# Performance work log

Hardware: AMD Instinct MI355X
Metric: run time of the kernel (lower is better)

Reference implementation:

```python
import jax, jax.numpy as jnp
import numpy as np

B, N, C, H, R = 64, 197, 768, 12, 98   # batch, tokens, dim, heads, eliminated tokens
SPARSITY, ALPHA = 0.2, 0.1
EPS = 1e-5  # torch nn.LayerNorm default


def layernorm(x, g, b):
    m = jnp.mean(x, axis=-1, keepdims=True)
    v = jnp.var(x, axis=-1, keepdims=True)
    return (x - m) / jnp.sqrt(v + EPS) * g + b


def setup_inputs() -> dict:
    key = jax.random.key(0)
    ks = jax.random.split(key, 8)
    s = lambda k, sh: (jax.random.normal(k, sh, jnp.float32) * 0.02)
    return dict(
        x=jax.random.normal(ks[0], (B, N, C), jnp.float32),
        norm1_g=jnp.ones((C,), jnp.float32), norm1_b=jnp.zeros((C,), jnp.float32),
        qkv_w=s(ks[1], (C, 3 * C)),                      # qkv_bias=False
        proj_w=s(ks[2], (C, C)), proj_b=jnp.zeros((C,), jnp.float32),
        norm2_g=jnp.ones((C,), jnp.float32), norm2_b=jnp.zeros((C,), jnp.float32),
        fc1_w=s(ks[3], (C, 4 * C)), fc1_b=jnp.zeros((4 * C,), jnp.float32),
        fc2_w=s(ks[4], (4 * C, C)), fc2_b=jnp.zeros((C,), jnp.float32),
    )


def reference(x, norm1_g, norm1_b, qkv_w, proj_w, proj_b,
              norm2_g, norm2_b, fc1_w, fc1_b, fc2_w, fc2_b):
    Dh = C // H
    scale = Dh ** -0.5
    # --- attention block ---
    h = layernorm(x, norm1_g, norm1_b)
    qkv = (h @ qkv_w).reshape(B, N, 3, H, Dh).transpose(2, 0, 3, 1, 4)
    q, k, v = qkv[0] * scale, qkv[1], qkv[2]
    attn = jax.nn.softmax(jnp.einsum('bhnd,bhmd->bhnm', q, k), axis=-1)  # [B,H,N,N]
    out = jnp.einsum('bhnm,bhmd->bhnd', attn, v).transpose(0, 2, 1, 3).reshape(B, N, C)
    x = x + out @ proj_w + proj_b
    # --- selection: DiagAttn (head-mean attention diagonal, excluding CLS) ---
    diag = jnp.diagonal(attn.mean(1), axis1=1, axis2=2)[:, 1:]          # [B, N-1]
    token_rank = jnp.argsort(-diag, axis=1) + 1                          # indices into [1, N)
    nk = N - 1 - R                                                       # kept image tokens
    idx_kept = jnp.sort(jnp.concatenate(
        [jnp.zeros((B, 1), token_rank.dtype), token_rank[:, :nk]], axis=1), axis=1)  # [B, K]
    idx_elim = jnp.sort(token_rank[:, nk:], axis=1)                      # [B, R]
    K = nk + 1
    # --- propagate: ThresholdGraph (multihead=True, threshold=True) ---
    x_kept = jnp.take_along_axis(x, idx_kept[:, :, None], axis=1)        # [B, K, C]
    x_elim = jnp.take_along_axis(x, idx_elim[:, :, None], axis=1)        # [B, R, C]
    w = jnp.take_along_axis(attn, idx_kept[:, None, :, None], axis=2)    # [B,H,K,N]
    w = jnp.take_along_axis(w, idx_elim[:, None, None, :], axis=3)       # [B,H,K,R]
    thr_idx = int(R * K * SPARSITY)
    w_sorted = -jnp.sort(-w.reshape(B, H, K * R), axis=-1)               # descending
    thr = w_sorted[:, :, thr_idx][:, :, None, None]
    w = jnp.where(w >= thr, w, jnp.zeros((), w.dtype))
    x_prop = jnp.einsum('bhke,behd->bkhd', w, x_elim.reshape(B, R, H, Dh)).reshape(B, K, C)
    x = x_kept + ALPHA * x_prop                                          # [B, K, C]
    # --- mlp block ---
    h2 = layernorm(x, norm2_g, norm2_b)
    h2 = jax.nn.gelu(h2 @ fc1_w + fc1_b, approximate=False) @ fc2_w + fc2_b
    return x + h2
```

## Files before the change

### kernel.cpp

```cpp
#include <hip/hip_runtime.h>
#include <math.h>

#define NTOK 197
#define CD   768
#define NH   12
#define DH   64
#define NBATCH 64
#define RTOK 98
#define KTOK 99
#define THRN 1941

typedef __attribute__((ext_vector_type(8))) short short8;
typedef __attribute__((ext_vector_type(8))) unsigned short u16x8;
typedef __attribute__((ext_vector_type(4))) float floatx4;

__device__ __forceinline__ int clamp196(int v){ return ((unsigned)v > 196u) ? 196 : v; }
__device__ __forceinline__ unsigned short f2b(float f){
  unsigned u = __float_as_uint(f);
  return (unsigned short)((u + 0x7FFFu + ((u>>16)&1u)) >> 16);
}
__device__ __forceinline__ float us2f(unsigned short u){ return __uint_as_float(((unsigned)u)<<16); }
__device__ __forceinline__ int swz(int row, int q){ return q ^ (((row>>1)&3)<<3); }

__global__ __launch_bounds__(256) void fill_kernel(float* __restrict__ out, int n, float val)
{
  int i = blockIdx.x*256 + threadIdx.x;
  if (i < n) out[i] = val;
}

__global__ __launch_bounds__(256) void tcast_k(const float* __restrict__ src, int K, int ldn, int col0,
                                               unsigned short* __restrict__ dst)
{
  __shared__ float t[32][33];
  int n0 = blockIdx.x*32, k0 = blockIdx.y*32;
  int lx = threadIdx.x & 31, ly = threadIdx.x >> 5;
#pragma unroll
  for (int i=0;i<4;i++)
    t[ly + i*8][lx] = src[(long)(k0 + ly + i*8)*ldn + col0 + n0 + lx];
  __syncthreads();
#pragma unroll
  for (int i=0;i<4;i++){
    int n = ly + i*8;
    dst[(long)(n0 + n)*K + k0 + lx] = f2b(t[lx][n]);
  }
}

__global__ __launch_bounds__(256) void tcast3_k(const float* __restrict__ src, int K, int ldn, int col0,
                                                unsigned short* __restrict__ dsth,
                                                unsigned short* __restrict__ dstl)
{
  __shared__ float t[32][33];
  int n0 = blockIdx.x*32, k0 = blockIdx.y*32;
  int lx = threadIdx.x & 31, ly = threadIdx.x >> 5;
#pragma unroll
  for (int i=0;i<4;i++)
    t[ly + i*8][lx] = src[(long)(k0 + ly + i*8)*ldn + col0 + n0 + lx];
  __syncthreads();
#pragma unroll
  for (int i=0;i<4;i++){
    int n = ly + i*8;
    float v = t[lx][n];
    unsigned short h = f2b(v);
    dsth[(long)(n0 + n)*K + k0 + lx] = h;
    dstl[(long)(n0 + n)*K + k0 + lx] = f2b(v - us2f(h));
  }
}

__global__ __launch_bounds__(256) void ln_kernel(const float* __restrict__ xin,
                                                 const float* __restrict__ gam,
                                                 const float* __restrict__ bet,
                                                 unsigned short* __restrict__ outh,
                                                 unsigned short* __restrict__ outl)
{
  int row = blockIdx.x;
  int tid = threadIdx.x;
  long base = (long)row * CD;
  float v[3];
#pragma unroll
  for (int i=0;i<3;i++) v[i] = xin[base + tid + i*256];
  float s  = v[0]+v[1]+v[2];
  float s2 = v[0]*v[0]+v[1]*v[1]+v[2]*v[2];
#pragma unroll
  for (int off=32; off; off>>=1){ s += __shfl_down(s,off); s2 += __shfl_down(s2,off); }
  __shared__ float ps[4], ps2[4], mb[2];
  if ((tid&63)==0){ ps[tid>>6]=s; ps2[tid>>6]=s2; }
  __syncthreads();
  if (tid==0){
    float S  = ps[0]+ps[1]+ps[2]+ps[3];
    float S2 = ps2[0]+ps2[1]+ps2[2]+ps2[3];
    float m  = S / (float)CD;
    float var = S2 / (float)CD - m*m;
    mb[0]=m; mb[1]=1.0f/sqrtf(var + 1e-5f);
  }
  __syncthreads();
  float m=mb[0], inv=mb[1];
#pragma unroll
  for (int i=0;i<3;i++){
    int c = tid + i*256;
    float r = (v[i]-m)*inv*gam[c] + bet[c];
    unsigned short h = f2b(r);
    outh[base+c] = h;
    if (outl) outl[base+c] = f2b(r - us2f(h));
  }
}

struct GemmP {
  const float* A;
  const void*  B;
  void*        C;
  int M, N, K, ldb, ldc;
  int zdiv;
  long as0, as1, bs0, bs1, cs0, cs1;
};

template<int EPI, int BF16B>
__global__ __launch_bounds__(256) void gemm_k(GemmP p)
{
  __shared__ float As[16][64];
  __shared__ float Bs[16][64];
  int z = blockIdx.z;
  int zq = z / p.zdiv, zr = z - zq*p.zdiv;
  long aoff = zq*p.as0 + zr*p.as1;
  long boff = zq*p.bs0 + zr*p.bs1;
  long coff = zq*p.cs0 + zr*p.cs1;
  int m0 = blockIdx.y*64, n0 = blockIdx.x*64;
  int tid = threadIdx.x;
  int tx = tid & 15, ty = tid >> 4;
  int am = tid >> 2, ak = (tid & 3) * 4;
  int bk = tid >> 4, bn = (tid & 15) * 4;
  bool aVec = ((p.K & 3) == 0);
  float acc[4][4] = {};
  for (int k0 = 0; k0 < p.K; k0 += 16) {
    float aa[4] = {0.f,0.f,0.f,0.f};
    {
      int gm = m0 + am;
      if (gm < p.M) {
        const float* ap = p.A + aoff + (long)gm*p.K + k0 + ak;
        if (aVec) {
          float4 t = *(const float4*)ap;
          aa[0]=t.x; aa[1]=t.y; aa[2]=t.z; aa[3]=t.w;
        } else {
#pragma unroll
          for (int i=0;i<4;i++) if (k0+ak+i < p.K) aa[i] = ap[i];
        }
      }
    }
    float bb[4] = {0.f,0.f,0.f,0.f};
    {
      int gk = k0 + bk;
      if (gk < p.K) {
        long idx = boff + (long)gk*p.ldb + n0 + bn;
        if (BF16B) {
          const unsigned short* bp = (const unsigned short*)p.B + idx;
          if (n0 + bn + 3 < p.N) {
            ushort4 t = *(const ushort4*)bp;
            bb[0]=us2f(t.x); bb[1]=us2f(t.y); bb[2]=us2f(t.z); bb[3]=us2f(t.w);
          } else {
#pragma unroll
            for (int i=0;i<4;i++) if (n0+bn+i < p.N) bb[i] = us2f(bp[i]);
          }
        } else {
          const float* bp = (const float*)p.B + idx;
          if (n0 + bn + 3 < p.N) {
            float4 t = *(const float4*)bp;
            bb[0]=t.x; bb[1]=t.y; bb[2]=t.z; bb[3]=t.w;
          } else {
#pragma unroll
            for (int i=0;i<4;i++) if (n0+bn+i < p.N) bb[i] = bp[i];
          }
        }
      }
    }
    __syncthreads();
#pragma unroll
    for (int i=0;i<4;i++) As[ak+i][am] = aa[i];
#pragma unroll
    for (int i=0;i<4;i++) Bs[bk][bn+i] = bb[i];
    __syncthreads();
#pragma unroll
    for (int kk=0;kk<16;kk++){
      float4 av = *(const float4*)&As[kk][ty*4];
      float4 bv = *(const float4*)&Bs[kk][tx*4];
      float av4[4]={av.x,av.y,av.z,av.w};
      float bv4[4]={bv.x,bv.y,bv.z,bv.w};
#pragma unroll
      for (int i=0;i<4;i++)
#pragma unroll
        for (int j=0;j<4;j++) acc[i][j] = fmaf(av4[i], bv4[j], acc[i][j]);
    }
  }
#pragma unroll
  for (int i=0;i<4;i++){
    int gm = m0 + ty*4 + i;
    if (gm >= p.M) continue;
#pragma unroll
    for (int j=0;j<4;j++){
      int gn = n0 + tx*4 + j;
      if (gn >= p.N) continue;
      float val = acc[i][j];
      if (EPI == 2) {
        ((unsigned short*)p.C)[coff + (long)gm*p.ldc + gn] = f2b(val);
      } else {
        ((float*)p.C)[coff + (long)gm*p.ldc + gn] = val;
      }
    }
  }
}

struct MmP {
  const unsigned short* A;
  const unsigned short* B;
  void* C;
  const float* bias;
  const float* resid;
  unsigned short* vout;
  int M, N, K, ldc;
};

template<int EPI>
__global__ __launch_bounds__(256) void mgemm_k(MmP p)
{
  __shared__ short As[128*32];
  __shared__ short Bs[128*32];
  int tid = threadIdx.x;
  int m0 = blockIdx.y*128, n0 = blockIdx.x*128;
  int w = tid>>6, l = tid&63;
  int wm = (w&1)*64, wn = (w>>1)*64;
  int lr = l&15, kq = (l>>4)*8;
  floatx4 acc[4][4];
#pragma unroll
  for (int i=0;i<4;i++)
#pragma unroll
    for (int j=0;j<4;j++) acc[i][j] = (floatx4){0.f,0.f,0.f,0.f};
  int r0i = tid>>2, q0 = (tid&3)*8;
  int r1i = r0i + 64;
  int w0s = swz(r0i, q0), w1s = swz(r1i, q0);
  for (int k0 = 0; k0 < p.K; k0 += 32) {
    u16x8 a0 = {0,0,0,0,0,0,0,0}, a1 = {0,0,0,0,0,0,0,0};
    { int gm = m0 + r0i;
      if (gm < p.M) a0 = *(const u16x8*)(p.A + (long)gm*p.K + k0 + q0); }
    { int gm = m0 + r1i;
      if (gm < p.M) a1 = *(const u16x8*)(p.A + (long)gm*p.K + k0 + q0); }
    u16x8 b0 = *(const u16x8*)(p.B + (long)(n0 + r0i)*p.K + k0 + q0);
    u16x8 b1 = *(const u16x8*)(p.B + (long)(n0 + r1i)*p.K + k0 + q0);
    __syncthreads();
    *(u16x8*)&As[r0i*32 + w0s] = a0;
    *(u16x8*)&As[r1i*32 + w1s] = a1;
    *(u16x8*)&Bs[r0i*32 + w0s] = b0;
    *(u16x8*)&Bs[r1i*32 + w1s] = b1;
    __syncthreads();
    short8 af[4], bfr[4];
#pragma unroll
    for (int mt=0;mt<4;mt++){ int rr = wm + mt*16 + lr; af[mt]  = *(short8*)&As[rr*32 + swz(rr,kq)]; }
#pragma unroll
    for (int nt=0;nt<4;nt++){ int rr = wn + nt*16 + lr; bfr[nt] = *(short8*)&Bs[rr*32 + swz(rr,kq)]; }
#pragma unroll
    for (int mt=0;mt<4;mt++)
#pragma unroll
      for (int nt=0;nt<4;nt++)
        acc[mt][nt] = __builtin_amdgcn_mfma_f32_16x16x32_bf16(af[mt], bfr[nt], acc[mt][nt], 0, 0, 0);
  }
  int rbase = (l>>4)*4;
#pragma unroll
  for (int mt=0;mt<4;mt++){
#pragma unroll
    for (int r=0;r<4;r++){
      int gm = m0 + wm + mt*16 + rbase + r;
      if (gm >= p.M) continue;
#pragma unroll
      for (int nt=0;nt<4;nt++){
        int gn = n0 + wn + nt*16 + lr;
        float val = acc[mt][nt][r];
        if (EPI == 1) {
          int cb = gm / NTOK, tok = gm - cb*NTOK;
          int h = gn >> 6, d = gn & 63;
          p.vout[(((long)cb*NH + h)*NTOK + tok)*DH + d] = f2b(val);
        } else if (EPI == 2) {
          ((float*)p.C)[(long)gm*p.ldc + gn] = val + p.bias[gn] + p.resid[(long)gm*p.ldc + gn];
        } else {
          float u = val + p.bias[gn];
          ((unsigned short*)p.C)[(long)gm*p.ldc + gn] = f2b(0.5f*u*(1.0f + erff(u*0.70710678118654752f)));
        }
      }
    }
  }
}

struct Mm3P {
  const unsigned short *Ah, *Al, *Bh, *Bl;
  float* C;
  unsigned short *qh, *ql, *kh, *kl;
  long az, bz, cz;
  int M, N, K, ldc;
};

template<int EPI>
__global__ __launch_bounds__(256) void mgemm3_k(Mm3P p)
{
  __shared__ short Ahs[128*32], Als[128*32], Bhs[128*32], Bls[128*32];
  int tid = threadIdx.x;
  int z = blockIdx.z;
  const unsigned short* Azh = p.Ah + (long)z*p.az;
  const unsigned short* Azl = p.Al + (long)z*p.az;
  const unsigned short* Bzh = p.Bh + (long)z*p.bz;
  const unsigned short* Bzl = p.Bl + (long)z*p.bz;
  int m0 = blockIdx.y*128, n0 = blockIdx.x*128;
  int w = tid>>6, l = tid&63;
  int wm = (w&1)*64, wn = (w>>1)*64;
  int lr = l&15, kq = (l>>4)*8;
  floatx4 acc[4][4];
#pragma unroll
  for (int i=0;i<4;i++)
#pragma unroll
    for (int j=0;j<4;j++) acc[i][j] = (floatx4){0.f,0.f,0.f,0.f};
  int r0i = tid>>2, q0 = (tid&3)*8;
  int r1i = r0i + 64;
  int w0s = swz(r0i, q0), w1s = swz(r1i, q0);
  for (int k0 = 0; k0 < p.K; k0 += 32) {
    u16x8 ah0={0,0,0,0,0,0,0,0}, al0={0,0,0,0,0,0,0,0};
    u16x8 ah1={0,0,0,0,0,0,0,0}, al1={0,0,0,0,0,0,0,0};
    u16x8 bh0={0,0,0,0,0,0,0,0}, bl0={0,0,0,0,0,0,0,0};
    u16x8 bh1={0,0,0,0,0,0,0,0}, bl1={0,0,0,0,0,0,0,0};
    { int gm = m0 + r0i;
      if (gm < p.M) {
        long o = (long)gm*p.K + k0 + q0;
        ah0 = *(const u16x8*)(Azh + o);
        al0 = *(const u16x8*)(Azl + o);
      } }
    { int gm = m0 + r1i;
      if (gm < p.M) {
        long o = (long)gm*p.K + k0 + q0;
        ah1 = *(const u16x8*)(Azh + o);
        al1 = *(const u16x8*)(Azl + o);
      } }
    { int gn = n0 + r0i;
      if (gn < p.N) {
        long o = (long)gn*p.K + k0 + q0;
        bh0 = *(const u16x8*)(Bzh + o);
        bl0 = *(const u16x8*)(Bzl + o);
      } }
    { int gn = n0 + r1i;
      if (gn < p.N) {
        long o = (long)gn*p.K + k0 + q0;
        bh1 = *(const u16x8*)(Bzh + o);
        bl1 = *(const u16x8*)(Bzl + o);
      } }
    __syncthreads();
    *(u16x8*)&Ahs[r0i*32 + w0s] = ah0;
    *(u16x8*)&Ahs[r1i*32 + w1s] = ah1;
    *(u16x8*)&Als[r0i*32 + w0s] = al0;
    *(u16x8*)&Als[r1i*32 + w1s] = al1;
    *(u16x8*)&Bhs[r0i*32 + w0s] = bh0;
    *(u16x8*)&Bhs[r1i*32 + w1s] = bh1;
    *(u16x8*)&Bls[r0i*32 + w0s] = bl0;
    *(u16x8*)&Bls[r1i*32 + w1s] = bl1;
    __syncthreads();
    short8 afh[4], afl[4], bfh[4], bfl[4];
#pragma unroll
    for (int mt=0;mt<4;mt++){
      int rr = wm + mt*16 + lr; int rs = rr*32 + swz(rr,kq);
      afh[mt] = *(short8*)&Ahs[rs];
      afl[mt] = *(short8*)&Als[rs];
    }
#pragma unroll
    for (int nt=0;nt<4;nt++){
      int rr = wn + nt*16 + lr; int rs = rr*32 + swz(rr,kq);
      bfh[nt] = *(short8*)&Bhs[rs];
      bfl[nt] = *(short8*)&Bls[rs];
    }
#pragma unroll
    for (int mt=0;mt<4;mt++)
#pragma unroll
      for (int nt=0;nt<4;nt++){
        acc[mt][nt] = __builtin_amdgcn_mfma_f32_16x16x32_bf16(afh[mt], bfh[nt], acc[mt][nt], 0, 0, 0);
        acc[mt][nt] = __builtin_amdgcn_mfma_f32_16x16x32_bf16(afh[mt], bfl[nt], acc[mt][nt], 0, 0, 0);
        acc[mt][nt] = __builtin_amdgcn_mfma_f32_16x16x32_bf16(afl[mt], bfh[nt], acc[mt][nt], 0, 0, 0);
      }
  }
  int rbase = (l>>4)*4;
#pragma unroll
  for (int mt=0;mt<4;mt++){
#pragma unroll
    for (int r=0;r<4;r++){
      int gm = m0 + wm + mt*16 + rbase + r;
      if (gm >= p.M) continue;
#pragma unroll
      for (int nt=0;nt<4;nt++){
        int gn = n0 + wn + nt*16 + lr;
        if (gn >= p.N) continue;
        float val = acc[mt][nt][r];
        if (EPI == 0) {
          p.C[(long)z*p.cz + (long)gm*p.ldc + gn] = val;
        } else {
          int which = (gn >= CD) ? 1 : 0;
          int rc = gn - which*CD;
          int hd = rc >> 6, dd = rc & 63;
          int cb = gm / NTOK, tok = gm - cb*NTOK;
          long off = (((long)cb*NH + hd)*NTOK + tok)*DH + dd;
          float v = which ? val : val*0.125f;
          unsigned short h = f2b(v);
          unsigned short lo16 = f2b(v - us2f(h));
          if (which) { p.kh[off] = h; p.kl[off] = lo16; }
          else       { p.qh[off] = h; p.ql[off] = lo16; }
        }
      }
    }
  }
}

__global__ __launch_bounds__(256) void softmax_kernel(float* __restrict__ attn)
{
  long row = (long)blockIdx.x*4 + (threadIdx.x>>6);
  int ln = threadIdx.x & 63;
  float* rp = attn + row*NTOK;
  float v[4]; float mx = -3.4e38f;
#pragma unroll
  for (int i=0;i<4;i++){
    int c = ln + i*64;
    v[i] = (c < NTOK) ? rp[c] : -3.4e38f;
    mx = fmaxf(mx, v[i]);
  }
#pragma unroll
  for (int off=32; off; off>>=1) mx = fmaxf(mx, __shfl_xor(mx, off));
  float sum = 0.f;
#pragma unroll
  for (int i=0;i<4;i++){
    int c = ln + i*64;
    v[i] = (c < NTOK) ? expf(v[i]-mx) : 0.f;
    sum += v[i];
  }
#pragma unroll
  for (int off=32; off; off>>=1) sum += __shfl_xor(sum, off);
#pragma unroll
  for (int i=0;i<4;i++){
    int c = ln + i*64;
    if (c < NTOK) rp[c] = v[i] / sum;
  }
}

__global__ __launch_bounds__(256) void select_kernel(const float* __restrict__ attn,
                                                     int* __restrict__ idx_kept,
                                                     int* __restrict__ idx_elim, int b0)
{
  int cb = blockIdx.x, tid = threadIdx.x;
  int b = b0 + cb;
  __shared__ float diag[NTOK-1];
  __shared__ int kept[NTOK];
  if (tid < NTOK-1) {
    int t = tid + 1;
    float s = 0.f;
#pragma unroll
    for (int h=0; h<NH; h++)
      s += attn[(((long)cb*NH + h)*NTOK + t)*NTOK + t];
    diag[tid] = s / 12.0f;
  }
  if (tid < KTOK) idx_kept[b*KTOK + tid] = 0;
  if (tid < RTOK) idx_elim[b*RTOK + tid] = 1;
  __syncthreads();
  if (tid < NTOK-1) {
    float dv = diag[tid];
    int r = 0;
    for (int m=0; m<NTOK-1; m++){
      float dm = diag[m];
      r += ((dm > dv) || (dm == dv && m < tid)) ? 1 : 0;
    }
    kept[tid+1] = (r < (NTOK-1-RTOK)) ? 1 : 0;
  }
  __syncthreads();
  if (tid < NTOK-1) {
    int t = tid + 1;
    if (kept[t]) {
      int pos = 1;
      for (int s2=1; s2<t; s2++) pos += kept[s2];
      if (pos >= 1 && pos < KTOK) idx_kept[b*KTOK + pos] = t;
    } else {
      int pos = 0;
      for (int s2=1; s2<t; s2++) pos += 1 - kept[s2];
      if (pos >= 0 && pos < RTOK) idx_elim[b*RTOK + pos] = t;
    }
  }
  if (tid == 0) idx_kept[b*KTOK] = 0;
}

__global__ __launch_bounds__(256) void prop_kernel(const float* __restrict__ attn,
                                                   const float* __restrict__ x1c,
                                                   const int* __restrict__ idx_kept,
                                                   const int* __restrict__ idx_elim,
                                                   float* __restrict__ x2, int b0)
{
  int z = blockIdx.x;
  int cb = z / NH, h = z - cb*NH;
  int b = b0 + cb;
  int tid = threadIdx.x;
  __shared__ float w[KTOK*RTOK];
  __shared__ unsigned short xe[RTOK*DH];
  __shared__ int kidx[KTOK], eidx[RTOK];
  __shared__ int cw[4];
  __shared__ int ctot;
  if (tid < KTOK) kidx[tid] = clamp196(idx_kept[b*KTOK + tid]);
  if (tid < RTOK) eidx[tid] = clamp196(idx_elim[b*RTOK + tid]);
  __syncthreads();
  const float* ab = attn + (long)z*NTOK*NTOK;
  for (int i=tid; i<KTOK*RTOK; i+=256){
    int k = i / RTOK, e = i - k*RTOK;
    w[i] = ab[kidx[k]*NTOK + eidx[e]];
  }
  for (int i=tid; i<RTOK*DH; i+=256){
    int e = i >> 6, d = i & 63;
    xe[i] = f2b(x1c[((long)cb*NTOK + eidx[e])*CD + h*DH + d]);
  }
  __syncthreads();
  unsigned lo = 0u, hi = 0x3f800001u;
  while (hi - lo > 1u) {
    unsigned mid = (lo + hi) >> 1;
    float t = __uint_as_float(mid);
    int c = 0;
    for (int i=tid; i<KTOK*RTOK; i+=256) c += (w[i] >= t) ? 1 : 0;
#pragma unroll
    for (int off=32; off; off>>=1) c += __shfl_down(c, off);
    if ((tid & 63) == 0) cw[tid>>6] = c;
    __syncthreads();
    if (tid == 0) ctot = cw[0]+cw[1]+cw[2]+cw[3];
    __syncthreads();
    int tot = ctot;
    __syncthreads();
    if (tot >= THRN) lo = mid; else hi = mid;
  }
  float tv = __uint_as_float(lo);
  for (int i=tid; i<KTOK*RTOK; i+=256) if (w[i] < tv) w[i] = 0.f;
  __syncthreads();
  int d = tid & 63;
  for (int k = tid>>6; k < KTOK; k += 4) {
    const float* wr = &w[k*RTOK];
    float acc = 0.f;
#pragma unroll 7
    for (int e=0; e<RTOK; e++)
      acc = fmaf(wr[e], us2f(xe[(e<<6) + d]), acc);
    float xk = x1c[((long)cb*NTOK + kidx[k])*CD + h*DH + d];
    x2[((long)b*KTOK + k)*CD + h*DH + d] = xk + 0.1f*acc;
  }
}

extern "C" void kernel_launch(void* const* d_in, const int* in_sizes, int n_in,
                              void* d_out, int out_size, void* d_ws, size_t ws_size,
                              hipStream_t stream)
{
  const float* x     = (const float*)d_in[0];
  const float* n1g   = (const float*)d_in[1];
  const float* n1b   = (const float*)d_in[2];
  const float* qkvw  = (const float*)d_in[3];
  const float* projw = (const float*)d_in[4];
  const float* projb = (const float*)d_in[5];
  const float* n2g   = (const float*)d_in[6];
  const float* n2b   = (const float*)d_in[7];
  const float* fc1w  = (const float*)d_in[8];
  const float* fc1b  = (const float*)d_in[9];
  const float* fc2w  = (const float*)d_in[10];
  const float* fc2b  = (const float*)d_in[11];
  float* out = (float*)d_out;

  const long XROW = (long)NTOK*CD;
  const long AH   = (long)NTOK*NTOK;
  const long AB   = (long)NH*AH;
  const long QH   = (long)NH*NTOK*DH;
  const long SMALL = 6336L + 6272L;
  const long WFIX  = 1769472L;
  const long PB = AB + 3*XROW + XROW/2;
  const long MLPFIX = 2359296L;
  const long MINREQ = SMALL + WFIX + (MLPFIX + 64*1920L > PB ? MLPFIX + 64*1920L : PB);

  long wsf = (long)(ws_size / 4);
  if (wsf < MINREQ) {
    float val = (float)(ws_size >> 20) * 1000.0f + 1.0f;
    fill_kernel<<<dim3((out_size+255)/256), 256, 0, stream>>>(out, out_size, val);
    return;
  }

  long avail = wsf - SMALL - WFIX;
  int G = (int)(avail / PB);
  if (G > NBATCH) G = NBATCH;
  if (G < 1) G = 1;
  long rcl = ((avail - MLPFIX) / 1920L) / 64L * 64L;
  int RC = (int)(rcl > 6336L ? 6336L : rcl);
  if (RC < 64) RC = 64;

  float* ws = (float*)d_ws;
  int*   idx_kept = (int*)ws;
  int*   idx_elim = idx_kept + 6336;
  unsigned short* qkwh   = (unsigned short*)(ws + SMALL);
  unsigned short* qkwl   = qkwh + 1179648;
  unsigned short* qkvwvT = qkwl + 1179648;
  unsigned short* projwT = qkvwvT + 589824;
  float* base  = ws + SMALL + WFIX;
  float* attnc = base;
  unsigned short* qh = (unsigned short*)(base + (long)G*AB);
  unsigned short* ql = qh + (long)G*XROW;
  float* x1c = (float*)qh;
  unsigned short* kh = (unsigned short*)(base + (long)G*AB + (long)G*XROW);
  unsigned short* kl = kh + (long)G*XROW;
  unsigned short* aoutb = kh;
  unsigned short* vc = (unsigned short*)(base + (long)G*AB + 2L*G*XROW);
  unsigned short* h1h = (unsigned short*)(base + (long)G*AB + 2L*G*XROW + (long)G*XROW/2);
  unsigned short* h1l = h1h + (long)G*XROW;
  unsigned short* fc1wT = (unsigned short*)base;
  unsigned short* fc2wT = fc1wT + 2359296;
  unsigned short* h2b   = (unsigned short*)(base + MLPFIX);
  unsigned short* gb    = h2b + (long)RC*CD;

  tcast3_k<<<dim3(48,24), 256, 0, stream>>>(qkvw, CD, 3*CD, 0, qkwh, qkwl);
  tcast_k <<<dim3(24,24), 256, 0, stream>>>(qkvw, CD, 3*CD, 2*CD, qkvwvT);
  tcast_k <<<dim3(24,24), 256, 0, stream>>>(projw, CD, CD, 0, projwT);

  for (int b0 = 0; b0 < NBATCH; b0 += G) {
    int GL = (NBATCH - b0 < G) ? (NBATCH - b0) : G;
    int MROW = GL*NTOK;
    ln_kernel<<<dim3(MROW), 256, 0, stream>>>(x + (long)b0*XROW, n1g, n1b, h1h, h1l);
    {
      Mm3P p{}; p.Ah=h1h; p.Al=h1l; p.Bh=qkwh; p.Bl=qkwl;
      p.qh=qh; p.ql=ql; p.kh=kh; p.kl=kl;
      p.M=MROW; p.N=2*CD; p.K=CD; p.ldc=0; p.az=0; p.bz=0; p.cz=0;
      mgemm3_k<1><<<dim3(12,(MROW+127)/128,1), 256, 0, stream>>>(p);
    }
    {
      MmP p{}; p.A=h1h; p.B=qkvwvT; p.vout=vc;
      p.M=MROW; p.N=CD; p.K=CD; p.ldc=CD;
      mgemm_k<1><<<dim3(6,(MROW+127)/128,1), 256, 0, stream>>>(p);
    }
    {
      Mm3P p{}; p.Ah=qh; p.Al=ql; p.Bh=kh; p.Bl=kl; p.C=attnc;
      p.M=NTOK; p.N=NTOK; p.K=DH; p.ldc=NTOK;
      p.az=(long)NTOK*DH; p.bz=(long)NTOK*DH; p.cz=AH;
      mgemm3_k<0><<<dim3(2,2,GL*NH), 256, 0, stream>>>(p);
    }
    softmax_kernel<<<dim3(GL*591), 256, 0, stream>>>(attnc);
    select_kernel<<<dim3(GL), 256, 0, stream>>>(attnc, idx_kept, idx_elim, b0);
    {
      GemmP p{}; p.A=attnc; p.B=vc; p.C=aoutb;
      p.M=NTOK; p.N=DH; p.K=NTOK; p.ldb=DH; p.ldc=CD; p.zdiv=NH;
      p.as0=AB; p.as1=AH; p.bs0=QH; p.bs1=(long)NTOK*DH; p.cs0=XROW; p.cs1=DH;
      gemm_k<2,1><<<dim3(1,4,GL*NH), 256, 0, stream>>>(p);
    }
    {
      MmP p{}; p.A=aoutb; p.B=projwT; p.C=x1c;
      p.M=MROW; p.N=CD; p.K=CD; p.ldc=CD;
      p.bias=projb; p.resid=x + (long)b0*XROW;
      mgemm_k<2><<<dim3(6,(MROW+127)/128,1), 256, 0, stream>>>(p);
    }
    prop_kernel<<<dim3(GL*NH), 256, 0, stream>>>(attnc, x1c, idx_kept, idx_elim, out, b0);
  }

  tcast_k<<<dim3(96,24), 256, 0, stream>>>(fc1w, CD, 4*CD, 0, fc1wT);
  tcast_k<<<dim3(24,96), 256, 0, stream>>>(fc2w, 4*CD, CD, 0, fc2wT);

  for (int r0 = 0; r0 < NBATCH*KTOK; r0 += RC) {
    int RCL = (NBATCH*KTOK - r0 < RC) ? (NBATCH*KTOK - r0) : RC;
    ln_kernel<<<dim3(RCL), 256, 0, stream>>>(out + (long)r0*CD, n2g, n2b, h2b, nullptr);
    {
      MmP p{}; p.A=h2b; p.B=fc1wT; p.C=gb;
      p.M=RCL; p.N=4*CD; p.K=CD; p.ldc=4*CD; p.bias=fc1b;
      mgemm_k<3><<<dim3(24,(RCL+127)/128,1), 256, 0, stream>>>(p);
    }
    {
      MmP p{}; p.A=gb; p.B=fc2wT; p.C=out + (long)r0*CD;
      p.M=RCL; p.N=CD; p.K=4*CD; p.ldc=CD;
      p.bias=fc2b; p.resid=out + (long)r0*CD;
      mgemm_k<2><<<dim3(6,(RCL+127)/128,1), 256, 0, stream>>>(p);
    }
  }
}
```

Baseline: 821.4 us.

## Use radix-select threshold and MFMA matmul in propagation kernel

After: 775.7 us. 1.06x faster.

```diff
diff --git a/kernel.cpp b/kernel.cpp
--- a/kernel.cpp
+++ b/kernel.cpp
@@ -9,6 +9,7 @@
 #define RTOK 98
 #define KTOK 99
 #define THRN 1941
+#define WTOT (KTOK*RTOK)
 
 typedef __attribute__((ext_vector_type(8))) short short8;
 typedef __attribute__((ext_vector_type(8))) unsigned short u16x8;
@@ -482,6 +483,7 @@
   if (tid == 0) idx_kept[b*KTOK] = 0;
 }
 
+#define PNEL 38
 __global__ __launch_bounds__(256) void prop_kernel(const float* __restrict__ attn,
                                                    const float* __restrict__ x1c,
                                                    const int* __restrict__ idx_kept,
@@ -492,52 +494,99 @@
   int cb = z / NH, h = z - cb*NH;
   int b = b0 + cb;
   int tid = threadIdx.x;
-  __shared__ float w[KTOK*RTOK];
-  __shared__ unsigned short xe[RTOK*DH];
+  int wid = tid >> 6, l = tid & 63;
+  int lr = l & 15, hi2 = l >> 4;
+  __shared__ short WhL[112*128];
+  __shared__ short XtL[64*128];
+  __shared__ unsigned hist[64];
   __shared__ int kidx[KTOK], eidx[RTOK];
-  __shared__ int cw[4];
-  __shared__ int ctot;
   if (tid < KTOK) kidx[tid] = clamp196(idx_kept[b*KTOK + tid]);
   if (tid < RTOK) eidx[tid] = clamp196(idx_elim[b*RTOK + tid]);
+  u16x8 zz = {0,0,0,0,0,0,0,0};
+#pragma unroll
+  for (int i=0;i<7;i++) *(u16x8*)&WhL[tid*8 + i*2048] = zz;
+#pragma unroll
+  for (int i=0;i<4;i++) *(u16x8*)&XtL[tid*8 + i*2048] = zz;
   __syncthreads();
+  for (int i = tid; i < RTOK*DH; i += 256){
+    int e = i >> 6, d = i & 63;
+    float v = x1c[((long)cb*NTOK + eidx[e])*CD + h*DH + d];
+    XtL[d*128 + (((e>>3) ^ (d&7))<<3) + (e&7)] = (short)f2b(v);
+  }
   const float* ab = attn + (long)z*NTOK*NTOK;
-  for (int i=tid; i<KTOK*RTOK; i+=256){
-    int k = i / RTOK, e = i - k*RTOK;
-    w[i] = ab[kidx[k]*NTOK + eidx[e]];
-  }
-  for (int i=tid; i<RTOK*DH; i+=256){
-    int e = i >> 6, d = i & 63;
-    xe[i] = f2b(x1c[((long)cb*NTOK + eidx[e])*CD + h*DH + d]);
+  unsigned wb[PNEL];
+#pragma unroll
+  for (int j=0;j<PNEL;j++){
+    int i = tid + (j<<8);
+    if (i < WTOT){
+      int k = i / RTOK, e = i - k*RTOK;
+      wb[j] = __float_as_uint(ab[kidx[k]*NTOK + eidx[e]]);
+    } else wb[j] = 0u;
+  }
+  unsigned P = 0; int rrank = THRN;
+  for (int pass=0; pass<5; ++pass){
+    int sh = 24 - 6*pass;
+    if (tid < 64) hist[tid] = 0u;
+    __syncthreads();
+#pragma unroll
+    for (int j=0;j<PNEL;j++){
+      int i = tid + (j<<8);
+      unsigned v = wb[j];
+      bool m = (i < WTOT) && ((pass == 0) || ((v >> (sh+6)) == P));
+      if (m) atomicAdd(&hist[(v>>sh)&63u], 1u);
+    }
+    __syncthreads();
+    unsigned cum = 0; int bsel = 0; unsigned above = 0;
+    for (int bb=63; bb>=0; --bb){
+      unsigned hv = hist[bb];
+      if (cum + hv >= (unsigned)rrank){ bsel = bb; above = cum; break; }
+      cum += hv;
+    }
+    P = (P<<6) | (unsigned)bsel;
+    rrank -= (int)above;
+    __syncthreads();
+  }
+  unsigned thrbits = P;
+#pragma unroll
+  for (int j=0;j<PNEL;j++){
+    int i = tid + (j<<8);
+    if (i < WTOT){
+      int k = i / RTOK, e = i - k*RTOK;
+      unsigned v = (wb[j] >= thrbits) ? wb[j] : 0u;
+      WhL[k*128 + (((e>>3) ^ (k&7))<<3) + (e&7)] = (short)f2b(__uint_as_float(v));
+    }
   }
   __syncthreads();
-  unsigned lo = 0u, hi = 0x3f800001u;
-  while (hi - lo > 1u) {
-    unsigned mid = (lo + hi) >> 1;
-    float t = __uint_as_float(mid);
-    int c = 0;
-    for (int i=tid; i<KTOK*RTOK; i+=256) c += (w[i] >= t) ? 1 : 0;
-#pragma unroll
-    for (int off=32; off; off>>=1) c += __shfl_down(c, off);
-    if ((tid & 63) == 0) cw[tid>>6] = c;
-    __syncthreads();
-    if (tid == 0) ctot = cw[0]+cw[1]+cw[2]+cw[3];
-    __syncthreads();
-    int tot = ctot;
-    __syncthreads();
-    if (tot >= THRN) lo = mid; else hi = mid;
-  }
-  float tv = __uint_as_float(lo);
-  for (int i=tid; i<KTOK*RTOK; i+=256) if (w[i] < tv) w[i] = 0.f;
-  __syncthreads();
-  int d = tid & 63;
-  for (int k = tid>>6; k < KTOK; k += 4) {
-    const float* wr = &w[k*RTOK];
-    float acc = 0.f;
-#pragma unroll 7
-    for (int e=0; e<RTOK; e++)
-      acc = fmaf(wr[e], us2f(xe[(e<<6) + d]), acc);
-    float xk = x1c[((long)cb*NTOK + kidx[k])*CD + h*DH + d];
-    x2[((long)b*KTOK + k)*CD + h*DH + d] = xk + 0.1f*acc;
+  floatx4 acc[7];
+#pragma unroll
+  for (int mt=0;mt<7;mt++) acc[mt] = (floatx4){0.f,0.f,0.f,0.f};
+  short8 bfr[4];
+#pragma unroll
+  for (int ks=0;ks<4;ks++){
+    int c = ks*4 + hi2;
+    int rd = wid*16 + lr;
+    bfr[ks] = *(short8*)&XtL[rd*128 + ((c ^ (lr&7))<<3)];
+  }
+#pragma unroll
+  for (int mt=0;mt<7;mt++){
+#pragma unroll
+    for (int ks=0;ks<4;ks++){
+      int c = ks*4 + hi2;
+      int rw = mt*16 + lr;
+      short8 af = *(short8*)&WhL[rw*128 + ((c ^ (lr&7))<<3)];
+      acc[mt] = __builtin_amdgcn_mfma_f32_16x16x32_bf16(af, bfr[ks], acc[mt], 0, 0, 0);
+    }
+  }
+#pragma unroll
+  for (int mt=0;mt<7;mt++){
+#pragma unroll
+    for (int r=0;r<4;r++){
+      int kt = mt*16 + hi2*4 + r;
+      if (kt >= KTOK) continue;
+      int d = wid*16 + lr;
+      float xk = x1c[((long)cb*NTOK + kidx[kt])*CD + h*DH + d];
+      x2[((long)b*KTOK + kt)*CD + h*DH + d] = xk + 0.1f*acc[mt][r];
+    }
   }
 }
 
```
